# Performance work log

Measured on AMD Instinct MI355X. Metric: run time of the kernel, lower is better.

## Reference

```python
import jax, jax.numpy as jnp
import numpy as np

HIDDEN = 1024
NUM_HEADS = 16
HEAD_DIM = HIDDEN // NUM_HEADS
B, S = 2, 2048


def setup_inputs() -> dict:
    key = jax.random.key(0)
    ks = jax.random.split(key, 7)
    scale = 1.0 / np.sqrt(HIDDEN)
    return {
        "hidden_states": jax.random.normal(ks[0], (B, S, HIDDEN), dtype=jnp.float32),
        "attention_mask": jnp.ones((B, S), dtype=jnp.float32),
        "Wq": jax.random.normal(ks[1], (HIDDEN, HIDDEN), dtype=jnp.float32) * scale,
        "bq": jax.random.normal(ks[2], (HIDDEN,), dtype=jnp.float32) * 0.02,
        "Wk": jax.random.normal(ks[3], (HIDDEN, HIDDEN), dtype=jnp.float32) * scale,
        "bk": jax.random.normal(ks[4], (HIDDEN,), dtype=jnp.float32) * 0.02,
        "Wv": jax.random.normal(ks[5], (HIDDEN, HIDDEN), dtype=jnp.float32) * scale,
        "bv": jax.random.normal(ks[6], (HIDDEN,), dtype=jnp.float32) * 0.02,
    }


def reference(hidden_states, attention_mask, Wq, bq, Wk, bk, Wv, bv):
    # Linear projections (W stored [in, out], equivalent to torch Linear).
    q = hidden_states @ Wq + bq  # [B,S,H]
    k = hidden_states @ Wk + bk
    v = hidden_states @ Wv + bv

    def split_heads(x):  # [B,S,H] -> [B,nh,S,hd]
        return x.reshape(B, S, NUM_HEADS, HEAD_DIM).transpose(0, 2, 1, 3)

    q, k, v = split_heads(q), split_heads(k), split_heads(v)

    scores = jnp.einsum("bhqd,bhkd->bhqk", q, k) / jnp.sqrt(
        jnp.asarray(HEAD_DIM, dtype=q.dtype))
    min_val = jnp.finfo(scores.dtype).min
    ext_mask = (1.0 - attention_mask[:, None, None, :]) * min_val  # [B,1,1,S]
    scores = scores + ext_mask
    probs = jax.nn.softmax(scores, axis=-1)  # eval mode: no dropout
    ctx = jnp.einsum("bhqk,bhkd->bhqd", probs, v)
    ctx = ctx.transpose(0, 2, 1, 3).reshape(B, S, HIDDEN)
    return ctx
```

## Files before the change

kernel.cpp:

```cpp
#include <hip/hip_runtime.h>
#include <hip/hip_bf16.h>
#include <cstddef>
#include <cstdint>

#define HID 1024
#define NHEADS 16
#define HDIM 64
#define BATCH 2
#define SEQ 2048
#define MROWS (BATCH * SEQ)
#define BHT (BATCH * NHEADS)

typedef __attribute__((ext_vector_type(8))) short s8v;
typedef __attribute__((ext_vector_type(4))) float f4v;
typedef __attribute__((ext_vector_type(2))) unsigned int u2v;

__device__ __forceinline__ unsigned int pkbf(float a, float b) {
    __hip_bfloat162 h = __float22bfloat162_rn(float2{a, b});
    union { __hip_bfloat162 v; unsigned int u; } c; c.v = h; return c.u;
}

__device__ __forceinline__ void lds_load16(void* lds, const void* g) {
    __builtin_amdgcn_global_load_lds(
        (const __attribute__((address_space(1))) void*)g,
        (__attribute__((address_space(3))) void*)lds, 16, 0, 0);
}

__global__ __launch_bounds__(256) void conv_fused_kernel(
    const float* __restrict__ hs, const float* __restrict__ mask,
    const float* __restrict__ Wq, const float* __restrict__ Wk,
    const float* __restrict__ Wv,
    unsigned short* __restrict__ Ah, unsigned short* __restrict__ WTh,
    float* __restrict__ lmask)
{
    if (blockIdx.x < 2048) {
        const int idx = (blockIdx.x * 256 + threadIdx.x) * 8;
        float4 v0 = *(const float4*)&hs[idx];
        float4 v1 = *(const float4*)&hs[idx + 4];
        union { unsigned int w[4]; } pk;
        pk.w[0] = pkbf(v0.x, v0.y);
        pk.w[1] = pkbf(v0.z, v0.w);
        pk.w[2] = pkbf(v1.x, v1.y);
        pk.w[3] = pkbf(v1.z, v1.w);
        *(uint4*)&Ah[idx] = *(uint4*)&pk;
    } else if (blockIdx.x < 2816) {
        const int bid = blockIdx.x - 2048;
        const int z = bid >> 8;
        const int rem = bid & 255;
        const float* W = (z == 0) ? Wq : (z == 1) ? Wk : Wv;
        unsigned short* th = WTh + (size_t)z * HID * HID;

        __shared__ float tile[64][65];
        const int t = threadIdx.x;
        const int kb = (rem >> 4) * 64, nb = (rem & 15) * 64;
        const int c4 = (t & 15) * 4;
        const int r0 = t >> 4;

#pragma unroll
        for (int i = 0; i < 4; ++i) {
            int r = r0 + i * 16;
            float4 v = *(const float4*)&W[(size_t)(kb + r) * HID + nb + c4];
            tile[r][c4 + 0] = v.x; tile[r][c4 + 1] = v.y;
            tile[r][c4 + 2] = v.z; tile[r][c4 + 3] = v.w;
        }
        __syncthreads();
#pragma unroll
        for (int i = 0; i < 4; ++i) {
            int n = r0 + i * 16;
            union { unsigned int w[2]; unsigned long long q; } pk;
            pk.w[0] = pkbf(tile[c4 + 0][n], tile[c4 + 1][n]);
            pk.w[1] = pkbf(tile[c4 + 2][n], tile[c4 + 3][n]);
            *(unsigned long long*)&th[(size_t)(nb + n) * HID + kb + c4] = pk.q;
        }
    } else {
        const int idx = (blockIdx.x - 2816) * 256 + threadIdx.x;
        lmask[idx] = (mask[idx] - 1.0f) * 1e30f;
    }
}

#define QSCALE 0.18033688011112042f

__global__ __launch_bounds__(256, 2) void qkv_mfma_kernel(
    const unsigned short* __restrict__ Ah, const unsigned short* __restrict__ WTh,
    const float* __restrict__ bq, const float* __restrict__ bk,
    const float* __restrict__ bv,
    unsigned short* __restrict__ Qg, unsigned short* __restrict__ Khi,
    unsigned short* __restrict__ VTg)
{
    __shared__ unsigned short S[32768];

    const int t = threadIdx.x;
    const int wave = t >> 6, lane = t & 63, quad = lane >> 4, l15 = lane & 15;
    const int sw = l15 & 7;
    const int wm = wave >> 1, wn = wave & 1;
    const int rowBase = blockIdx.x * 128;
    const int yb = blockIdx.y;
    const int colBase = yb * 128;

    const int srow8 = lane >> 3;
    const int sc    = lane & 7;
    size_t goffA[4], goffB[4];
#pragma unroll
    for (int it = 0; it < 4; ++it) {
        const int row = (wave * 4 + it) * 8 + srow8;
        const int gx = (sc ^ (row & 7)) * 8;
        goffA[it] = (size_t)(rowBase + row) * HID + gx;
        goffB[it] = (size_t)(colBase + row) * HID + gx;
    }

    f4v acc[4][4];
#pragma unroll
    for (int mf = 0; mf < 4; ++mf)
#pragma unroll
        for (int nf = 0; nf < 4; ++nf) acc[mf][nf] = (f4v){0.f, 0.f, 0.f, 0.f};

#pragma unroll
    for (int it = 0; it < 4; ++it) {
        lds_load16(&S[(wave * 4 + it) * 512], &Ah[goffA[it]]);
        lds_load16(&S[8192 + (wave * 4 + it) * 512], &WTh[goffB[it]]);
    }
    __syncthreads();

    const bool isQK = (yb < 16);

    for (int kt = 0; kt < HID / 64; ++kt) {
        const int cur = (kt & 1) << 14;
        const int nxt = cur ^ 16384;
        if (kt < HID / 64 - 1) {
            const int k0 = (kt + 1) * 64;
#pragma unroll
            for (int it = 0; it < 4; ++it) {
                lds_load16(&S[nxt + (wave * 4 + it) * 512], &Ah[goffA[it] + k0]);
                lds_load16(&S[nxt + 8192 + (wave * 4 + it) * 512], &WTh[goffB[it] + k0]);
            }
        }
        const unsigned short* AS = &S[cur];
        const unsigned short* BS = &S[cur + 8192];
#pragma unroll
        for (int kk = 0; kk < 2; ++kk) {
            const int csw = ((kk * 4 + quad) ^ sw) * 8;
            s8v af[4], bf[4];
#pragma unroll
            for (int mf = 0; mf < 4; ++mf)
                af[mf] = *(const s8v*)&AS[(wm * 64 + mf * 16 + l15) * 64 + csw];
#pragma unroll
            for (int nf = 0; nf < 4; ++nf)
                bf[nf] = *(const s8v*)&BS[(wn * 64 + nf * 16 + l15) * 64 + csw];
            if (isQK) {
#pragma unroll
                for (int mf = 0; mf < 4; ++mf)
#pragma unroll
                    for (int nf = 0; nf < 4; ++nf)
                        acc[mf][nf] = __builtin_amdgcn_mfma_f32_16x16x32_bf16(bf[nf], af[mf], acc[mf][nf], 0, 0, 0);
            } else {
#pragma unroll
                for (int mf = 0; mf < 4; ++mf)
#pragma unroll
                    for (int nf = 0; nf < 4; ++nf)
                        acc[mf][nf] = __builtin_amdgcn_mfma_f32_16x16x32_bf16(af[mf], bf[nf], acc[mf][nf], 0, 0, 0);
            }
        }
        __syncthreads();
    }

    if (yb < 8) {
#pragma unroll
        for (int nf = 0; nf < 4; ++nf) {
            const int n0 = colBase + wn * 64 + nf * 16 + quad * 4;
            const float4 bb = *(const float4*)&bq[n0];
            const int h = n0 >> 6, d0 = n0 & 63;
#pragma unroll
            for (int mf = 0; mf < 4; ++mf) {
                const int rw = rowBase + wm * 64 + mf * 16 + l15;
                const int b = rw >> 11;
                const int ss = rw & (SEQ - 1);
                union { unsigned int w[2]; unsigned long long q; } pk;
                pk.w[0] = pkbf((acc[mf][nf][0] + bb.x) * QSCALE, (acc[mf][nf][1] + bb.y) * QSCALE);
                pk.w[1] = pkbf((acc[mf][nf][2] + bb.z) * QSCALE, (acc[mf][nf][3] + bb.w) * QSCALE);
                *(unsigned long long*)&Qg[((size_t)(b * NHEADS + h) * SEQ + ss) * HDIM + d0] = pk.q;
            }
        }
    } else if (yb < 16) {
#pragma unroll
        for (int nf = 0; nf < 4; ++nf) {
            const int nk = colBase - 1024 + wn * 64 + nf * 16 + quad * 4;
            const float4 bb = *(const float4*)&bk[nk];
            const int h = nk >> 6, d0 = nk & 63;
#pragma unroll
            for (int mf = 0; mf < 4; ++mf) {
                const int rw = rowBase + wm * 64 + mf * 16 + l15;
                const int b = rw >> 11;
                const int ss = rw & (SEQ - 1);
                union { unsigned int w[2]; unsigned long long q; } pk;
                pk.w[0] = pkbf(acc[mf][nf][0] + bb.x, acc[mf][nf][1] + bb.y);
                pk.w[1] = pkbf(acc[mf][nf][2] + bb.z, acc[mf][nf][3] + bb.w);
                *(unsigned long long*)&Khi[((size_t)(b * NHEADS + h) * SEQ + ss) * HDIM + d0] = pk.q;
            }
        }
    } else {
#pragma unroll
        for (int nf = 0; nf < 4; ++nf) {
            const int nv = colBase - 2048 + wn * 64 + nf * 16 + l15;
            const float bb = bv[nv];
            const int h = nv >> 6, d = nv & 63;
#pragma unroll
            for (int mf = 0; mf < 4; ++mf) {
                const int rw0 = rowBase + wm * 64 + mf * 16 + quad * 4;
                const int b = rw0 >> 11;
                const int s0 = rw0 & (SEQ - 1);
                union { unsigned int w[2]; unsigned long long q; } pk;
                pk.w[0] = pkbf(acc[mf][nf][0] + bb, acc[mf][nf][1] + bb);
                pk.w[1] = pkbf(acc[mf][nf][2] + bb, acc[mf][nf][3] + bb);
                *(unsigned long long*)&VTg[((size_t)(b * NHEADS + h) * HDIM + d) * SEQ + s0] = pk.q;
            }
        }
    }
}

#define BC 64
#define NT (SEQ / BC)

__global__ __launch_bounds__(256, 4) void attn_mfma_kernel(
    const unsigned short* __restrict__ Qg, const unsigned short* __restrict__ Khi,
    const unsigned short* __restrict__ VTg,
    const float* __restrict__ lmask, float* __restrict__ out)
{
    __shared__ unsigned short Kb[2][BC * HDIM];
    __shared__ unsigned short Vb[2][BC * HDIM];

    const int t = threadIdx.x;
    const int wave = t >> 6, lane = t & 63, quad = lane >> 4, l15 = lane & 15;
    const int sw = l15 & 7;
    const int bh = blockIdx.x, b = bh >> 4, h = bh & (NHEADS - 1);
    const int qbase = blockIdx.y * 128 + wave * 32;

    const size_t hb = (size_t)bh * SEQ * HDIM;
    const unsigned short* kbase = Khi + hb;
    const unsigned short* vbase = VTg + hb;
    const float* mrow = lmask + b * SEQ;

    s8v qh[2][2];
#pragma unroll
    for (int qf = 0; qf < 2; ++qf)
#pragma unroll
        for (int ds = 0; ds < 2; ++ds) {
            size_t off = hb + (size_t)(qbase + qf * 16 + l15) * HDIM + ds * 32 + quad * 8;
            qh[qf][ds] = *(const s8v*)&Qg[off];
        }

    s8v ones;
#pragma unroll
    for (int j = 0; j < 8; ++j) ones[j] = (short)0x3F80;

    f4v oacc[2][4], lacc[2];
#pragma unroll
    for (int qf = 0; qf < 2; ++qf) {
#pragma unroll
        for (int nf = 0; nf < 4; ++nf) oacc[qf][nf] = (f4v){0.f, 0.f, 0.f, 0.f};
        lacc[qf] = (f4v){0.f, 0.f, 0.f, 0.f};
    }

    const int srow8 = lane >> 3;
    const int sc    = lane & 7;
    int koff[2], voff[2];
#pragma unroll
    for (int it = 0; it < 2; ++it) {
        const int row = (wave * 2 + it) * 8 + srow8;
        const int gx = (sc ^ (row & 7)) * 8;
        koff[it] = row * HDIM + gx;
        voff[it] = row * SEQ + gx;
    }

#pragma unroll
    for (int it = 0; it < 2; ++it) {
        const int i = wave * 2 + it;
        lds_load16(&Kb[0][i * 512], kbase + koff[it]);
        lds_load16(&Vb[0][i * 512], vbase + voff[it]);
    }
    __syncthreads();

    for (int kt = 0; kt < NT; ++kt) {
        const int cur = kt & 1;
        if (kt + 1 < NT) {
            const int nxt = cur ^ 1;
#pragma unroll
            for (int it = 0; it < 2; ++it) {
                const int i = wave * 2 + it;
                lds_load16(&Kb[nxt][i * 512], kbase + (kt + 1) * BC * HDIM + koff[it]);
                lds_load16(&Vb[nxt][i * 512], vbase + (kt + 1) * BC + voff[it]);
            }
        }

        float4 msv[4];
#pragma unroll
        for (int mf = 0; mf < 4; ++mf)
            msv[mf] = *(const float4*)&mrow[kt * BC + mf * 16 + quad * 4];

        f4v sacc[2][4];
#pragma unroll
        for (int qf = 0; qf < 2; ++qf)
#pragma unroll
            for (int mf = 0; mf < 4; ++mf)
                sacc[qf][mf] = (f4v){msv[mf].x, msv[mf].y, msv[mf].z, msv[mf].w};

        __builtin_amdgcn_s_setprio(1);
#pragma unroll
        for (int mf = 0; mf < 4; ++mf) {
#pragma unroll
            for (int ds = 0; ds < 2; ++ds) {
                s8v kh = *(const s8v*)&Kb[cur][(mf * 16 + l15) * HDIM + (((ds * 4 + quad) ^ sw) * 8)];
#pragma unroll
                for (int qf = 0; qf < 2; ++qf)
                    sacc[qf][mf] = __builtin_amdgcn_mfma_f32_16x16x32_bf16(kh, qh[qf][ds], sacc[qf][mf], 0, 0, 0);
            }
        }
        __builtin_amdgcn_s_setprio(0);

        s8v pa[2][2];
#pragma unroll
        for (int qf = 0; qf < 2; ++qf) {
            unsigned int wlo[4], whi[4];
#pragma unroll
            for (int mf = 0; mf < 4; ++mf) {
                float e0 = __builtin_amdgcn_exp2f(sacc[qf][mf][0]);
                float e1 = __builtin_amdgcn_exp2f(sacc[qf][mf][1]);
                float e2 = __builtin_amdgcn_exp2f(sacc[qf][mf][2]);
                float e3 = __builtin_amdgcn_exp2f(sacc[qf][mf][3]);
                wlo[mf] = pkbf(e0, e1);
                whi[mf] = pkbf(e2, e3);
            }
#pragma unroll
            for (int ks = 0; ks < 2; ++ks) {
                unsigned int alo = wlo[ks * 2], blo = wlo[ks * 2 + 1];
                unsigned int ahi = whi[ks * 2], bhi = whi[ks * 2 + 1];
                u2v r;
                r = __builtin_amdgcn_permlane32_swap(alo, blo, false, false); alo = r[0]; blo = r[1];
                r = __builtin_amdgcn_permlane32_swap(ahi, bhi, false, false); ahi = r[0]; bhi = r[1];
                r = __builtin_amdgcn_permlane16_swap(alo, blo, false, false); alo = r[0]; blo = r[1];
                r = __builtin_amdgcn_permlane16_swap(ahi, bhi, false, false); ahi = r[0]; bhi = r[1];
                union { unsigned int w[4]; s8v v; } up;
                up.w[0] = alo; up.w[1] = ahi; up.w[2] = blo; up.w[3] = bhi;
                pa[qf][ks] = up.v;
            }
        }

        __builtin_amdgcn_s_setprio(1);
#pragma unroll
        for (int ks = 0; ks < 2; ++ks) {
            const int csw = ((ks * 4 + quad) ^ sw) * 8;
#pragma unroll
            for (int nf = 0; nf < 4; ++nf) {
                s8v vb = *(const s8v*)&Vb[cur][(nf * 16 + l15) * BC + csw];
                oacc[0][nf] = __builtin_amdgcn_mfma_f32_16x16x32_bf16(pa[0][ks], vb, oacc[0][nf], 0, 0, 0);
                oacc[1][nf] = __builtin_amdgcn_mfma_f32_16x16x32_bf16(pa[1][ks], vb, oacc[1][nf], 0, 0, 0);
            }
            lacc[0] = __builtin_amdgcn_mfma_f32_16x16x32_bf16(pa[0][ks], ones, lacc[0], 0, 0, 0);
            lacc[1] = __builtin_amdgcn_mfma_f32_16x16x32_bf16(pa[1][ks], ones, lacc[1], 0, 0, 0);
        }
        __builtin_amdgcn_s_setprio(0);
        __syncthreads();
    }

#pragma unroll
    for (int qf = 0; qf < 2; ++qf) {
        float lv[4];
#pragma unroll
        for (int r = 0; r < 4; ++r) lv[r] = 1.0f / lacc[qf][r];
#pragma unroll
        for (int nf = 0; nf < 4; ++nf)
#pragma unroll
            for (int r = 0; r < 4; ++r) {
                int q = qbase + qf * 16 + quad * 4 + r;
                int d = nf * 16 + l15;
                out[((size_t)b * SEQ + q) * HID + h * HDIM + d] = oacc[qf][nf][r] * lv[r];
            }
    }
}

extern "C" void kernel_launch(void* const* d_in, const int* in_sizes, int n_in,
                              void* d_out, int out_size, void* d_ws, size_t ws_size,
                              hipStream_t stream) {
    const float* hs   = (const float*)d_in[0];
    const float* mask = (const float*)d_in[1];
    const float* Wq   = (const float*)d_in[2];
    const float* bq   = (const float*)d_in[3];
    const float* Wk   = (const float*)d_in[4];
    const float* bk   = (const float*)d_in[5];
    const float* Wv   = (const float*)d_in[6];
    const float* bv   = (const float*)d_in[7];
    float* out = (float*)d_out;

    const size_t N = (size_t)MROWS * HID;
    unsigned short* Qg  = (unsigned short*)d_ws;
    unsigned short* Khi = Qg + N;
    unsigned short* VTg = Qg + 2 * N;
    unsigned short* Ah  = Qg + 3 * N;
    unsigned short* WTh = Qg + 4 * N;
    float* lmask = (float*)(WTh + (size_t)3 * HID * HID);

    conv_fused_kernel<<<2048 + 768 + 16, 256, 0, stream>>>(hs, mask, Wq, Wk, Wv, Ah, WTh, lmask);

    dim3 g1(MROWS / 128, 3 * HID / 128);
    qkv_mfma_kernel<<<g1, 256, 0, stream>>>(Ah, WTh, bq, bk, bv, Qg, Khi, VTg);

    dim3 g2(BHT, SEQ / 128);
    attn_mfma_kernel<<<g2, 256, 0, stream>>>(Qg, Khi, VTg, lmask, out);
}
```

Baseline: 164.1 us.

## Fold mask into V and row-sum, double query rows per attention wave

The additive mask bias in the score accumulators is replaced by multiplying V by the mask in the projection epilogue and using a bf16 mask vector instead of ones for the row-sum MFMA. This removes per-tile float mask loads and accumulator initialisation. Each wave now processes 64 query rows, doubling reuse of each K/V LDS tile and halving the grid. The cost is much higher register use and lower occupancy, and exactness depends on the mask being 0/1 valued.

```diff
diff --git a/kernel.cpp b/kernel.cpp
--- a/kernel.cpp
+++ b/kernel.cpp
@@ -31,7 +31,7 @@
     const float* __restrict__ Wq, const float* __restrict__ Wk,
     const float* __restrict__ Wv,
     unsigned short* __restrict__ Ah, unsigned short* __restrict__ WTh,
-    float* __restrict__ lmask)
+    unsigned short* __restrict__ maskbf)
 {
     if (blockIdx.x < 2048) {
         const int idx = (blockIdx.x * 256 + threadIdx.x) * 8;
@@ -74,7 +74,9 @@
         }
     } else {
         const int idx = (blockIdx.x - 2816) * 256 + threadIdx.x;
-        lmask[idx] = (mask[idx] - 1.0f) * 1e30f;
+        union { unsigned int u; unsigned short s[2]; } cv;
+        cv.u = pkbf(mask[idx], 0.f);
+        maskbf[idx] = cv.s[0];
     }
 }
 
@@ -83,7 +85,7 @@
 __global__ __launch_bounds__(256, 2) void qkv_mfma_kernel(
     const unsigned short* __restrict__ Ah, const unsigned short* __restrict__ WTh,
     const float* __restrict__ bq, const float* __restrict__ bk,
-    const float* __restrict__ bv,
+    const float* __restrict__ bv, const float* __restrict__ mask,
     unsigned short* __restrict__ Qg, unsigned short* __restrict__ Khi,
     unsigned short* __restrict__ VTg)
 {
@@ -208,9 +210,10 @@
                 const int rw0 = rowBase + wm * 64 + mf * 16 + quad * 4;
                 const int b = rw0 >> 11;
                 const int s0 = rw0 & (SEQ - 1);
+                const float4 mv = *(const float4*)&mask[b * SEQ + s0];
                 union { unsigned int w[2]; unsigned long long q; } pk;
-                pk.w[0] = pkbf(acc[mf][nf][0] + bb, acc[mf][nf][1] + bb);
-                pk.w[1] = pkbf(acc[mf][nf][2] + bb, acc[mf][nf][3] + bb);
+                pk.w[0] = pkbf((acc[mf][nf][0] + bb) * mv.x, (acc[mf][nf][1] + bb) * mv.y);
+                pk.w[1] = pkbf((acc[mf][nf][2] + bb) * mv.z, (acc[mf][nf][3] + bb) * mv.w);
                 *(unsigned long long*)&VTg[((size_t)(b * NHEADS + h) * HDIM + d) * SEQ + s0] = pk.q;
             }
         }
@@ -220,10 +223,10 @@
 #define BC 64
 #define NT (SEQ / BC)
 
-__global__ __launch_bounds__(256, 4) void attn_mfma_kernel(
+__global__ __launch_bounds__(256, 1) void attn_mfma_kernel(
     const unsigned short* __restrict__ Qg, const unsigned short* __restrict__ Khi,
     const unsigned short* __restrict__ VTg,
-    const float* __restrict__ lmask, float* __restrict__ out)
+    const unsigned short* __restrict__ maskbf, float* __restrict__ out)
 {
     __shared__ unsigned short Kb[2][BC * HDIM];
     __shared__ unsigned short Vb[2][BC * HDIM];
@@ -232,29 +235,25 @@
     const int wave = t >> 6, lane = t & 63, quad = lane >> 4, l15 = lane & 15;
     const int sw = l15 & 7;
     const int bh = blockIdx.x, b = bh >> 4, h = bh & (NHEADS - 1);
-    const int qbase = blockIdx.y * 128 + wave * 32;
+    const int qbase = blockIdx.y * 256 + wave * 64;
 
     const size_t hb = (size_t)bh * SEQ * HDIM;
     const unsigned short* kbase = Khi + hb;
     const unsigned short* vbase = VTg + hb;
-    const float* mrow = lmask + b * SEQ;
-
-    s8v qh[2][2];
-#pragma unroll
-    for (int qf = 0; qf < 2; ++qf)
+    const unsigned short* mrow = maskbf + b * SEQ;
+
+    s8v qh[4][2];
+#pragma unroll
+    for (int qf = 0; qf < 4; ++qf)
 #pragma unroll
         for (int ds = 0; ds < 2; ++ds) {
             size_t off = hb + (size_t)(qbase + qf * 16 + l15) * HDIM + ds * 32 + quad * 8;
             qh[qf][ds] = *(const s8v*)&Qg[off];
         }
 
-    s8v ones;
-#pragma unroll
-    for (int j = 0; j < 8; ++j) ones[j] = (short)0x3F80;
-
-    f4v oacc[2][4], lacc[2];
-#pragma unroll
-    for (int qf = 0; qf < 2; ++qf) {
+    f4v oacc[4][4], lacc[4];
+#pragma unroll
+    for (int qf = 0; qf < 4; ++qf) {
 #pragma unroll
         for (int nf = 0; nf < 4; ++nf) oacc[qf][nf] = (f4v){0.f, 0.f, 0.f, 0.f};
         lacc[qf] = (f4v){0.f, 0.f, 0.f, 0.f};
@@ -291,17 +290,15 @@
             }
         }
 
-        float4 msv[4];
-#pragma unroll
-        for (int mf = 0; mf < 4; ++mf)
-            msv[mf] = *(const float4*)&mrow[kt * BC + mf * 16 + quad * 4];
-
-        f4v sacc[2][4];
-#pragma unroll
-        for (int qf = 0; qf < 2; ++qf)
+        s8v mb0 = *(const s8v*)&mrow[kt * BC + quad * 8];
+        s8v mb1 = *(const s8v*)&mrow[kt * BC + 32 + quad * 8];
+
+        f4v sacc[4][4];
+#pragma unroll
+        for (int qf = 0; qf < 4; ++qf)
 #pragma unroll
             for (int mf = 0; mf < 4; ++mf)
-                sacc[qf][mf] = (f4v){msv[mf].x, msv[mf].y, msv[mf].z, msv[mf].w};
+                sacc[qf][mf] = (f4v){0.f, 0.f, 0.f, 0.f};
 
         __builtin_amdgcn_s_setprio(1);
 #pragma unroll
@@ -310,15 +307,15 @@
             for (int ds = 0; ds < 2; ++ds) {
                 s8v kh = *(const s8v*)&Kb[cur][(mf * 16 + l15) * HDIM + (((ds * 4 + quad) ^ sw) * 8)];
 #pragma unroll
-                for (int qf = 0; qf < 2; ++qf)
+                for (int qf = 0; qf < 4; ++qf)
                     sacc[qf][mf] = __builtin_amdgcn_mfma_f32_16x16x32_bf16(kh, qh[qf][ds], sacc[qf][mf], 0, 0, 0);
             }
         }
         __builtin_amdgcn_s_setprio(0);
 
-        s8v pa[2][2];
-#pragma unroll
-        for (int qf = 0; qf < 2; ++qf) {
+        s8v pa[4][2];
+#pragma unroll
+        for (int qf = 0; qf < 4; ++qf) {
             unsigned int wlo[4], whi[4];
 #pragma unroll
             for (int mf = 0; mf < 4; ++mf) {
@@ -351,18 +348,21 @@
 #pragma unroll
             for (int nf = 0; nf < 4; ++nf) {
                 s8v vb = *(const s8v*)&Vb[cur][(nf * 16 + l15) * BC + csw];
-                oacc[0][nf] = __builtin_amdgcn_mfma_f32_16x16x32_bf16(pa[0][ks], vb, oacc[0][nf], 0, 0, 0);
-                oacc[1][nf] = __builtin_amdgcn_mfma_f32_16x16x32_bf16(pa[1][ks], vb, oacc[1][nf], 0, 0, 0);
-            }
-            lacc[0] = __builtin_amdgcn_mfma_f32_16x16x32_bf16(pa[0][ks], ones, lacc[0], 0, 0, 0);
-            lacc[1] = __builtin_amdgcn_mfma_f32_16x16x32_bf16(pa[1][ks], ones, lacc[1], 0, 0, 0);
+#pragma unroll
+                for (int qf = 0; qf < 4; ++qf)
+                    oacc[qf][nf] = __builtin_amdgcn_mfma_f32_16x16x32_bf16(pa[qf][ks], vb, oacc[qf][nf], 0, 0, 0);
+            }
+            const s8v mb = ks ? mb1 : mb0;
+#pragma unroll
+            for (int qf = 0; qf < 4; ++qf)
+                lacc[qf] = __builtin_amdgcn_mfma_f32_16x16x32_bf16(pa[qf][ks], mb, lacc[qf], 0, 0, 0);
         }
         __builtin_amdgcn_s_setprio(0);
         __syncthreads();
     }
 
 #pragma unroll
-    for (int qf = 0; qf < 2; ++qf) {
+    for (int qf = 0; qf < 4; ++qf) {
         float lv[4];
 #pragma unroll
         for (int r = 0; r < 4; ++r) lv[r] = 1.0f / lacc[qf][r];
@@ -396,13 +396,13 @@
     unsigned short* VTg = Qg + 2 * N;
     unsigned short* Ah  = Qg + 3 * N;
     unsigned short* WTh = Qg + 4 * N;
-    float* lmask = (float*)(WTh + (size_t)3 * HID * HID);
-
-    conv_fused_kernel<<<2048 + 768 + 16, 256, 0, stream>>>(hs, mask, Wq, Wk, Wv, Ah, WTh, lmask);
+    unsigned short* maskbf = WTh + (size_t)3 * HID * HID;
+
+    conv_fused_kernel<<<2048 + 768 + 16, 256, 0, stream>>>(hs, mask, Wq, Wk, Wv, Ah, WTh, maskbf);
 
     dim3 g1(MROWS / 128, 3 * HID / 128);
-    qkv_mfma_kernel<<<g1, 256, 0, stream>>>(Ah, WTh, bq, bk, bv, Qg, Khi, VTg);
-
-    dim3 g2(BHT, SEQ / 128);
-    attn_mfma_kernel<<<g2, 256, 0, stream>>>(Qg, Khi, VTg, lmask, out);
-}
+    qkv_mfma_kernel<<<g1, 256, 0, stream>>>(Ah, WTh, bq, bk, bv, mask, Qg, Khi, VTg);
+
+    dim3 g2(BHT, SEQ / 256);
+    attn_mfma_kernel<<<g2, 256, 0, stream>>>(Qg, Khi, VTg, maskbf, out);
+}
```

Measured after the change: 182.7 us. +11.3%, slower.
